# Kernel optimization log

Measured on AMD Instinct MI355X. Metric: run time of the kernel, lower is better.

## Reference

```python
import jax, jax.numpy as jnp
import numpy as np

B, S, D, H, L, F = 4, 2048, 512, 8, 4, 2048
DH = D // H
EPS = 1e-5


def setup_inputs() -> dict:
    key = jax.random.key(0)
    ks = jax.random.split(key, 16)
    sc = 0.02
    inp = {
        "turn_embeddings": jax.random.normal(ks[0], (B, S, D), jnp.float32),
        "Wqkv": jax.random.normal(ks[1], (L, 3 * D, D), jnp.float32) * sc,
        "bqkv": jnp.zeros((L, 3 * D), jnp.float32),
        "Wo": jax.random.normal(ks[2], (L, D, D), jnp.float32) * sc,
        "bo": jnp.zeros((L, D), jnp.float32),
        "W1": jax.random.normal(ks[3], (L, F, D), jnp.float32) * sc,
        "b1": jnp.zeros((L, F), jnp.float32),
        "W2": jax.random.normal(ks[4], (L, D, F), jnp.float32) * sc,
        "b2": jnp.zeros((L, D), jnp.float32),
        "ln1_g": jnp.ones((L, D), jnp.float32),
        "ln1_b": jnp.zeros((L, D), jnp.float32),
        "ln2_g": jnp.ones((L, D), jnp.float32),
        "ln2_b": jnp.zeros((L, D), jnp.float32),
        "speaker_ids": jax.random.randint(ks[5], (B, S), 0, 4, jnp.int64 if jax.config.jax_enable_x64 else jnp.int32),
    }
    return inp


def _layer_norm(x, g, b):
    mu = jnp.mean(x, axis=-1, keepdims=True)
    var = jnp.mean(jnp.square(x - mu), axis=-1, keepdims=True)
    return (x - mu) * jax.lax.rsqrt(var + EPS) * g + b


def _attention(x, Wqkv, bqkv, Wo, bo, allow):
    # x: [B,S,D]; allow: [B,1,S,S] boolean (causal & same-speaker)
    qkv = x @ Wqkv.T + bqkv                       # [B,S,3D]
    q, k, v = jnp.split(qkv, 3, axis=-1)
    q = q.reshape(x.shape[0], x.shape[1], H, DH)
    k = k.reshape(x.shape[0], x.shape[1], H, DH)
    v = v.reshape(x.shape[0], x.shape[1], H, DH)
    scores = jnp.einsum("bqhd,bkhd->bhqk", q, k) / np.sqrt(DH)
    scores = jnp.where(allow, scores, jnp.finfo(scores.dtype).min)
    p = jax.nn.softmax(scores, axis=-1)
    o = jnp.einsum("bhqk,bkhd->bqhd", p, v).reshape(x.shape[0], x.shape[1], D)
    return o @ Wo.T + bo


def reference(turn_embeddings, Wqkv, bqkv, Wo, bo, W1, b1, W2, b2,
              ln1_g, ln1_b, ln2_g, ln2_b, speaker_ids):
    Bc, Sc, _ = turn_embeddings.shape
    causal = jnp.tril(jnp.ones((Sc, Sc), bool))                 # [S,S]
    same = speaker_ids[:, :, None] == speaker_ids[:, None, :]    # [B,S,S]
    allow = (same & causal)[:, None, :, :]                       # [B,1,S,S]
    x = turn_embeddings
    for l in range(L):
        a = _attention(x, Wqkv[l], bqkv[l], Wo[l], bo[l], allow)
        x = _layer_norm(x + a, ln1_g[l], ln1_b[l])
        h = jax.nn.relu(x @ W1[l].T + b1[l]) @ W2[l].T + b2[l]
        x = _layer_norm(x + h, ln2_g[l], ln2_b[l])
    return x
```

## Files before the change

kernel.cpp:

```cpp
#include <hip/hip_runtime.h>
#include <stdint.h>

#define BN 4
#define SN 2048
#define DN 512
#define HN 8
#define LN 4
#define FN 2048
#define MN (BN * SN)
#define TD (3 * DN)

typedef __attribute__((ext_vector_type(8))) __bf16 bf16x8;
typedef __attribute__((ext_vector_type(4))) float f32x4;
typedef __attribute__((ext_vector_type(8))) unsigned short ushortx8;

static __device__ __forceinline__ unsigned short f2bf(float f) {
    return __builtin_bit_cast(unsigned short, (__bf16)f);
}
static __device__ __forceinline__ float bf2f(unsigned short h) {
    return __builtin_bit_cast(float, (uint32_t)h << 16);
}

static __device__ __forceinline__ void gload16(const void* g, void* l) {
    __builtin_amdgcn_global_load_lds(
        (const __attribute__((address_space(1))) void*)g,
        (__attribute__((address_space(3))) void*)l, 16, 0, 0);
}

__global__ __launch_bounds__(256) void k_cvt(const float* __restrict__ src,
                                             unsigned short* __restrict__ dst,
                                             int n4) {
    int i = blockIdx.x * blockDim.x + threadIdx.x;
    int stride = gridDim.x * blockDim.x;
    for (; i < n4; i += stride) {
        float4 v = ((const float4*)src)[i];
        ushort4 o;
        o.x = f2bf(v.x); o.y = f2bf(v.y); o.z = f2bf(v.z); o.w = f2bf(v.w);
        ((ushort4*)dst)[i] = o;
    }
}

template <int MODE, int BNT>
__global__ __launch_bounds__(256) void k_gemm(const unsigned short* __restrict__ A,
                                              const unsigned short* __restrict__ B,
                                              const float* __restrict__ bias,
                                              unsigned short* __restrict__ Cb,
                                              int M, int N, int K, int GX) {
    __shared__ __align__(16) unsigned short As[128][64];
    __shared__ __align__(16) unsigned short Bs[BNT][64];
    constexpr int NFR = BNT / 32;

    const int t = threadIdx.x;
    const int lane = t & 63;
    const int wid = t >> 6;
    const int wm = wid >> 1, wn = wid & 1;
    const int lr = lane & 15;
    const int lg = lane >> 4;

    const int nwg = gridDim.x;
    const int bid = blockIdx.x;
    const int swz = (bid & 7) * (nwg >> 3) + (bid >> 3);
    const int bx = swz % GX;
    const int by = swz / GX;

    const size_t rowA = (size_t)by * 128;
    const size_t rowB = (size_t)bx * BNT;
    const unsigned short* Ab = A + rowA * K;
    const unsigned short* Bb = B + rowB * K;

    const int srow = lane >> 3;
    const int sgran = (lane & 7) ^ srow;

    f32x4 acc[4][NFR] = {};

    for (int k0 = 0; k0 < K; k0 += 64) {
        __syncthreads();
#pragma unroll
        for (int j = 0; j < 4; ++j) {
            const int c = wid * 4 + j;
            const size_t goff = (size_t)(8 * c + srow) * K + k0 + sgran * 8;
            gload16(Ab + goff, &As[8 * c][0]);
        }
#pragma unroll
        for (int j = 0; j < NFR; ++j) {
            const int c = wid * NFR + j;
            const size_t goff = (size_t)(8 * c + srow) * K + k0 + sgran * 8;
            gload16(Bb + goff, &Bs[8 * c][0]);
        }
        __syncthreads();

#pragma unroll
        for (int h = 0; h < 2; ++h) {
            const int gp = (h * 4 + lg) ^ (lr & 7);
            bf16x8 af[4], bfr[NFR];
#pragma unroll
            for (int mi = 0; mi < 4; ++mi)
                af[mi] = *(const bf16x8*)&As[wm * 64 + mi * 16 + lr][gp * 8];
#pragma unroll
            for (int ni = 0; ni < NFR; ++ni)
                bfr[ni] = *(const bf16x8*)&Bs[wn * (BNT / 2) + ni * 16 + lr][gp * 8];
#pragma unroll
            for (int mi = 0; mi < 4; ++mi)
#pragma unroll
                for (int ni = 0; ni < NFR; ++ni)
                    acc[mi][ni] = __builtin_amdgcn_mfma_f32_16x16x32_bf16(
                        af[mi], bfr[ni], acc[mi][ni], 0, 0, 0);
        }
    }

    float bv[NFR];
#pragma unroll
    for (int ni = 0; ni < NFR; ++ni)
        bv[ni] = bias[(int)rowB + wn * (BNT / 2) + ni * 16 + lr];

#pragma unroll
    for (int mi = 0; mi < 4; ++mi) {
#pragma unroll
        for (int ni = 0; ni < NFR; ++ni) {
            int col = (int)rowB + wn * (BNT / 2) + ni * 16 + lr;
            int row0 = (int)rowA + wm * 64 + mi * 16 + lg * 4;
#pragma unroll
            for (int r = 0; r < 4; ++r) {
                float v = acc[mi][ni][r] + bv[ni];
                if (MODE == 2) v = fmaxf(v, 0.f);
                Cb[(size_t)(row0 + r) * N + col] = f2bf(v);
            }
        }
    }
}

__global__ __launch_bounds__(256) void k_attn(const unsigned short* __restrict__ qkv,
                                              const int* __restrict__ spk,
                                              unsigned short* __restrict__ o) {
    __shared__ __align__(16) unsigned short Ks[2][64][64];
    __shared__ __align__(16) unsigned short Vt[2][64][64];
    __shared__ __align__(16) unsigned short Ps[4][16][64];

    const int t = threadIdx.x;
    const int lane = t & 63;
    const int w = t >> 6;
    const int lr = lane & 15;
    const int lg = lane >> 4;
    const int l7 = lr & 7;

    const int wg = blockIdx.x;
    const int inner = wg >> 3;
    const int bh = 4 * (wg & 7) + (inner & 3);
    const int qtile = (SN / 64 - 1) - (inner >> 2);
    const int b = bh >> 3;
    const int h = bh & 7;
    const int qb = qtile * 64;

    const size_t base = (size_t)b * SN * TD;
    const unsigned short* kg = qkv + base + DN + h * 64;
    const unsigned short* vg = qkv + base + 2 * DN + h * 64;

    const float SCL = 0.125f * 1.4426950408889634f;
    const unsigned short* qptr = qkv + base + (size_t)(qb + w * 16 + lr) * TD + h * 64;
    bf16x8 aq0 = *(const bf16x8*)(qptr + lg * 8);
    bf16x8 aq1 = *(const bf16x8*)(qptr + 32 + lg * 8);
#pragma unroll
    for (int j = 0; j < 8; ++j) {
        aq0[j] = (__bf16)((float)aq0[j] * SCL);
        aq1[j] = (__bf16)((float)aq1[j] * SCL);
    }

    int sqr[4], qrow[4];
#pragma unroll
    for (int r = 0; r < 4; ++r) {
        qrow[r] = qb + w * 16 + lg * 4 + r;
        sqr[r] = spk[b * SN + qrow[r]];
    }

    const int kr0 = t >> 3;
    const int kgr = ((t & 7) ^ (kr0 & 7)) * 8;
    const int vrow = t & 63;
    const int vd0 = (t >> 6) * 16;

    uint4 kra = *(const uint4*)&kg[(size_t)kr0 * TD + (t & 7) * 8];
    uint4 krb = *(const uint4*)&kg[(size_t)(kr0 + 32) * TD + (t & 7) * 8];
    ushortx8 vra = *(const ushortx8*)&vg[(size_t)vrow * TD + vd0];
    ushortx8 vrb = *(const ushortx8*)&vg[(size_t)vrow * TD + vd0 + 8];
    *(uint4*)&Ks[0][kr0][kgr] = kra;
    *(uint4*)&Ks[0][kr0 + 32][kgr] = krb;
#pragma unroll
    for (int j = 0; j < 8; ++j) {
        const int vcol = (((vrow >> 3) ^ j) << 3) + (vrow & 7);
        Vt[0][vd0 + j][vcol] = vra[j];
        Vt[0][vd0 + 8 + j][vcol] = vrb[j];
    }

    float lsum[4] = {0.f, 0.f, 0.f, 0.f};
    f32x4 acc_o[4] = {};

    const int ntiles = qtile + 1;
    for (int it = 0; it < ntiles; ++it) {
        const int k0 = it * 64;
        const int cur = it & 1;
        __syncthreads();

        const bool nx = (it + 1 < ntiles);
        if (nx) {
            const int kn = k0 + 64;
            kra = *(const uint4*)&kg[(size_t)(kn + kr0) * TD + (t & 7) * 8];
            krb = *(const uint4*)&kg[(size_t)(kn + kr0 + 32) * TD + (t & 7) * 8];
            vra = *(const ushortx8*)&vg[(size_t)(kn + vrow) * TD + vd0];
            vrb = *(const ushortx8*)&vg[(size_t)(kn + vrow) * TD + vd0 + 8];
        }
        int skr[4];
#pragma unroll
        for (int ni = 0; ni < 4; ++ni) skr[ni] = spk[b * SN + k0 + 16 * ni + lr];

        f32x4 sc4[4] = {};
        __builtin_amdgcn_s_setprio(1);
#pragma unroll
        for (int ni = 0; ni < 4; ++ni) {
            bf16x8 bk0 = *(const bf16x8*)&Ks[cur][16 * ni + lr][(lg ^ l7) * 8];
            bf16x8 bk1 = *(const bf16x8*)&Ks[cur][16 * ni + lr][((lg + 4) ^ l7) * 8];
            sc4[ni] = __builtin_amdgcn_mfma_f32_16x16x32_bf16(aq0, bk0, sc4[ni], 0, 0, 0);
            sc4[ni] = __builtin_amdgcn_mfma_f32_16x16x32_bf16(aq1, bk1, sc4[ni], 0, 0, 0);
        }
        __builtin_amdgcn_s_setprio(0);

        const bool diag = (it == ntiles - 1);
#pragma unroll
        for (int ni = 0; ni < 4; ++ni) {
#pragma unroll
            for (int r = 0; r < 4; ++r) {
                bool allow = (skr[ni] == sqr[r]);
                if (diag) allow = allow && (16 * ni + lr <= w * 16 + lg * 4 + r);
                float p = allow ? __builtin_amdgcn_exp2f(sc4[ni][r]) : 0.f;
                lsum[r] += p;
                const int q7 = (lg * 4 + r) & 7;
                const int pg = ((2 * ni + (lr >> 3)) ^ q7) * 8 + l7;
                Ps[w][lg * 4 + r][pg] = f2bf(p);
            }
        }

        bf16x8 ap0 = *(const bf16x8*)&Ps[w][lr][(lg ^ l7) * 8];
        bf16x8 ap1 = *(const bf16x8*)&Ps[w][lr][((lg + 4) ^ l7) * 8];
        __builtin_amdgcn_s_setprio(1);
#pragma unroll
        for (int ni = 0; ni < 4; ++ni) {
            bf16x8 bv0 = *(const bf16x8*)&Vt[cur][16 * ni + lr][(lg ^ l7) * 8];
            bf16x8 bv1 = *(const bf16x8*)&Vt[cur][16 * ni + lr][((lg + 4) ^ l7) * 8];
            acc_o[ni] = __builtin_amdgcn_mfma_f32_16x16x32_bf16(ap0, bv0, acc_o[ni], 0, 0, 0);
            acc_o[ni] = __builtin_amdgcn_mfma_f32_16x16x32_bf16(ap1, bv1, acc_o[ni], 0, 0, 0);
        }
        __builtin_amdgcn_s_setprio(0);

        if (nx) {
            const int nb = cur ^ 1;
            *(uint4*)&Ks[nb][kr0][kgr] = kra;
            *(uint4*)&Ks[nb][kr0 + 32][kgr] = krb;
#pragma unroll
            for (int j = 0; j < 8; ++j) {
                const int vcol = (((vrow >> 3) ^ j) << 3) + (vrow & 7);
                Vt[nb][vd0 + j][vcol] = vra[j];
                Vt[nb][vd0 + 8 + j][vcol] = vrb[j];
            }
        }
    }

#pragma unroll
    for (int r = 0; r < 4; ++r) {
        float s = lsum[r];
        s += __shfl_xor(s, 1);
        s += __shfl_xor(s, 2);
        s += __shfl_xor(s, 4);
        s += __shfl_xor(s, 8);
        float inv = 1.f / s;
#pragma unroll
        for (int ni = 0; ni < 4; ++ni) {
            int d = 16 * ni + lr;
            o[(size_t)(b * SN + qrow[r]) * DN + h * 64 + d] = f2bf(acc_o[ni][r] * inv);
        }
    }
}

template <bool XF32>
__global__ __launch_bounds__(256) void k_add_ln(const void* __restrict__ xin_,
                                                const unsigned short* __restrict__ dl,
                                                const float* __restrict__ g,
                                                const float* __restrict__ bta,
                                                unsigned short* __restrict__ xb,
                                                float* __restrict__ fout) {
    const int row = blockIdx.x * 4 + (threadIdx.x >> 6);
    const int lane = threadIdx.x & 63;
    const size_t off = (size_t)row * DN + lane * 8;
    const int c0 = lane * 8;

    float v[8];
    if (XF32) {
        const float* xin = (const float*)xin_;
        float4 a0 = *(const float4*)&xin[off];
        float4 a1 = *(const float4*)&xin[off + 4];
        v[0] = a0.x; v[1] = a0.y; v[2] = a0.z; v[3] = a0.w;
        v[4] = a1.x; v[5] = a1.y; v[6] = a1.z; v[7] = a1.w;
    } else {
        ushortx8 xa = *(const ushortx8*)&((const unsigned short*)xin_)[off];
#pragma unroll
        for (int i = 0; i < 8; ++i) v[i] = bf2f(xa[i]);
    }
    ushortx8 dd = *(const ushortx8*)&dl[off];
#pragma unroll
    for (int i = 0; i < 8; ++i) v[i] += bf2f(dd[i]);

    float s1 = 0.f, s2 = 0.f;
#pragma unroll
    for (int i = 0; i < 8; ++i) { s1 += v[i]; s2 += v[i] * v[i]; }
#pragma unroll
    for (int msk = 32; msk; msk >>= 1) {
        s1 += __shfl_xor(s1, msk);
        s2 += __shfl_xor(s2, msk);
    }
    const float mean = s1 * (1.f / 512.f);
    const float var = s2 * (1.f / 512.f) - mean * mean;
    const float rs = rsqrtf(var + 1e-5f);

    float4 g0 = *(const float4*)&g[c0];
    float4 g1 = *(const float4*)&g[c0 + 4];
    float4 b0 = *(const float4*)&bta[c0];
    float4 b1 = *(const float4*)&bta[c0 + 4];
    float gg[8] = {g0.x, g0.y, g0.z, g0.w, g1.x, g1.y, g1.z, g1.w};
    float bb[8] = {b0.x, b0.y, b0.z, b0.w, b1.x, b1.y, b1.z, b1.w};

    float y[8];
    ushortx8 ub;
#pragma unroll
    for (int i = 0; i < 8; ++i) {
        y[i] = (v[i] - mean) * rs * gg[i] + bb[i];
        ub[i] = f2bf(y[i]);
    }
    *(ushortx8*)&xb[off] = ub;
    if (fout) {
        *(float4*)&fout[off] = make_float4(y[0], y[1], y[2], y[3]);
        *(float4*)&fout[off + 4] = make_float4(y[4], y[5], y[6], y[7]);
    }
}

extern "C" void kernel_launch(void* const* d_in, const int* in_sizes, int n_in,
                              void* d_out, int out_size, void* d_ws, size_t ws_size,
                              hipStream_t stream) {
    const float* te   = (const float*)d_in[0];
    const float* Wqkv = (const float*)d_in[1];
    const float* bqkv = (const float*)d_in[2];
    const float* Wo   = (const float*)d_in[3];
    const float* bo   = (const float*)d_in[4];
    const float* W1   = (const float*)d_in[5];
    const float* b1   = (const float*)d_in[6];
    const float* W2   = (const float*)d_in[7];
    const float* b2   = (const float*)d_in[8];
    const float* g1   = (const float*)d_in[9];
    const float* be1  = (const float*)d_in[10];
    const float* g2   = (const float*)d_in[11];
    const float* be2  = (const float*)d_in[12];
    const int*   spk  = (const int*)d_in[13];
    float* out = (float*)d_out;

    char* ws = (char*)d_ws;
    size_t off = 0;
    auto alloc = [&](size_t bytes) -> char* {
        char* p = ws + off;
        off += (bytes + 255) & ~(size_t)255;
        return p;
    };
    unsigned short* wqkv_b = (unsigned short*)alloc((size_t)LN * TD * DN * 2);
    unsigned short* wo_b   = (unsigned short*)alloc((size_t)LN * DN * DN * 2);
    unsigned short* w1_b   = (unsigned short*)alloc((size_t)LN * FN * DN * 2);
    unsigned short* w2_b   = (unsigned short*)alloc((size_t)LN * DN * FN * 2);
    unsigned short* xb     = (unsigned short*)alloc((size_t)MN * DN * 2);
    unsigned short* u      = (unsigned short*)alloc((size_t)MN * FN * 2);
    unsigned short* ob     = (unsigned short*)alloc((size_t)MN * DN * 2);
    unsigned short* projb  = (unsigned short*)alloc((size_t)MN * DN * 2);
    unsigned short* qkvb = u;
    unsigned short* hb   = u;

    k_cvt<<<2048, 256, 0, stream>>>(Wqkv, wqkv_b, LN * TD * DN / 4);
    k_cvt<<<2048, 256, 0, stream>>>(Wo,   wo_b,   LN * DN * DN / 4);
    k_cvt<<<2048, 256, 0, stream>>>(W1,   w1_b,   LN * FN * DN / 4);
    k_cvt<<<2048, 256, 0, stream>>>(W2,   w2_b,   LN * DN * FN / 4);
    k_cvt<<<2048, 256, 0, stream>>>(te,   xb,     MN * DN / 4);

    for (int l = 0; l < LN; ++l) {
        k_gemm<1, 128><<<(MN / 128) * (TD / 128), 256, 0, stream>>>(
            xb, wqkv_b + (size_t)l * TD * DN, bqkv + l * TD, qkvb,
            MN, TD, DN, TD / 128);
        k_attn<<<(SN / 64) * BN * HN, 256, 0, stream>>>(qkvb, spk, ob);
        k_gemm<1, 64><<<(MN / 128) * (DN / 64), 256, 0, stream>>>(
            ob, wo_b + (size_t)l * DN * DN, bo + l * DN, projb,
            MN, DN, DN, DN / 64);
        if (l == 0)
            k_add_ln<true><<<MN / 4, 256, 0, stream>>>(
                te, projb, g1 + l * DN, be1 + l * DN, xb, nullptr);
        else
            k_add_ln<false><<<MN / 4, 256, 0, stream>>>(
                xb, projb, g1 + l * DN, be1 + l * DN, xb, nullptr);
        k_gemm<2, 128><<<(MN / 128) * (FN / 128), 256, 0, stream>>>(
            xb, w1_b + (size_t)l * FN * DN, b1 + l * FN, hb,
            MN, FN, DN, FN / 128);
        k_gemm<1, 64><<<(MN / 128) * (DN / 64), 256, 0, stream>>>(
            hb, w2_b + (size_t)l * DN * FN, b2 + l * DN, projb,
            MN, DN, FN, DN / 64);
        k_add_ln<false><<<MN / 4, 256, 0, stream>>>(
            xb, projb, g2 + l * DN, be2 + l * DN, xb,
            (l == LN - 1) ? out : nullptr);
    }
    (void)in_sizes; (void)n_in; (void)out_size; (void)ws_size;
}
```

Before: 606.3 us.

## Widen attention blocks to 128 queries with 8 waves and fuse weight conversions

The attention kernel now runs 512 threads per block covering 128 query rows, so each K/V tile loaded into LDS is shared by twice as many waves, and the grid is halved. K tiles are fetched with direct global-to-LDS loads, speaker ids are cached in LDS as bytes, and waves skip key tiles that lie entirely past their causal limit. The five fp32-to-bf16 conversion launches are merged into one kernel with range dispatch. Costs include larger blocks with per-wave load imbalance on the diagonal tiles, and fewer blocks to spread across the compute units.

```diff
diff --git a/kernel.cpp b/kernel.cpp
--- a/kernel.cpp
+++ b/kernel.cpp
@@ -27,16 +27,34 @@
         (__attribute__((address_space(3))) void*)l, 16, 0, 0);
 }
 
-__global__ __launch_bounds__(256) void k_cvt(const float* __restrict__ src,
-                                             unsigned short* __restrict__ dst,
-                                             int n4) {
+__global__ __launch_bounds__(256) void k_cvt_all(const float* __restrict__ Wqkv,
+                                                 const float* __restrict__ Wo,
+                                                 const float* __restrict__ W1,
+                                                 const float* __restrict__ W2,
+                                                 const float* __restrict__ te,
+                                                 unsigned short* __restrict__ wqkv_b,
+                                                 unsigned short* __restrict__ wo_b,
+                                                 unsigned short* __restrict__ w1_b,
+                                                 unsigned short* __restrict__ w2_b,
+                                                 unsigned short* __restrict__ xb) {
+    constexpr int G0 = LN * TD * DN / 4;
+    constexpr int G1 = G0 + LN * DN * DN / 4;
+    constexpr int G2 = G1 + LN * FN * DN / 4;
+    constexpr int G3 = G2 + LN * DN * FN / 4;
+    constexpr int G4 = G3 + MN * DN / 4;
     int i = blockIdx.x * blockDim.x + threadIdx.x;
     int stride = gridDim.x * blockDim.x;
-    for (; i < n4; i += stride) {
-        float4 v = ((const float4*)src)[i];
+    for (; i < G4; i += stride) {
+        const float* s; unsigned short* d; int j;
+        if (i < G0)      { s = Wqkv; d = wqkv_b; j = i; }
+        else if (i < G1) { s = Wo;   d = wo_b;   j = i - G0; }
+        else if (i < G2) { s = W1;   d = w1_b;   j = i - G1; }
+        else if (i < G3) { s = W2;   d = w2_b;   j = i - G2; }
+        else             { s = te;   d = xb;     j = i - G3; }
+        float4 v = ((const float4*)s)[j];
         ushort4 o;
         o.x = f2bf(v.x); o.y = f2bf(v.y); o.z = f2bf(v.z); o.w = f2bf(v.w);
-        ((ushort4*)dst)[i] = o;
+        ((ushort4*)d)[j] = o;
     }
 }
 
@@ -129,12 +147,13 @@
     }
 }
 
-__global__ __launch_bounds__(256) void k_attn(const unsigned short* __restrict__ qkv,
+__global__ __launch_bounds__(512) void k_attn(const unsigned short* __restrict__ qkv,
                                               const int* __restrict__ spk,
                                               unsigned short* __restrict__ o) {
     __shared__ __align__(16) unsigned short Ks[2][64][64];
     __shared__ __align__(16) unsigned short Vt[2][64][64];
-    __shared__ __align__(16) unsigned short Ps[4][16][64];
+    __shared__ __align__(16) unsigned short Ps[8][16][64];
+    __shared__ unsigned char skb[SN];
 
     const int t = threadIdx.x;
     const int lane = t & 63;
@@ -146,14 +165,16 @@
     const int wg = blockIdx.x;
     const int inner = wg >> 3;
     const int bh = 4 * (wg & 7) + (inner & 3);
-    const int qtile = (SN / 64 - 1) - (inner >> 2);
+    const int qsuper = (SN / 128 - 1) - (inner >> 2);
     const int b = bh >> 3;
     const int h = bh & 7;
-    const int qb = qtile * 64;
+    const int qb = qsuper * 128;
 
     const size_t base = (size_t)b * SN * TD;
     const unsigned short* kg = qkv + base + DN + h * 64;
     const unsigned short* vg = qkv + base + 2 * DN + h * 64;
+
+    for (int i = t; i < SN; i += 512) skb[i] = (unsigned char)spk[b * SN + i];
 
     const float SCL = 0.125f * 1.4426950408889634f;
     const unsigned short* qptr = qkv + base + (size_t)(qb + w * 16 + lr) * TD + h * 64;
@@ -172,28 +193,24 @@
         sqr[r] = spk[b * SN + qrow[r]];
     }
 
-    const int kr0 = t >> 3;
-    const int kgr = ((t & 7) ^ (kr0 & 7)) * 8;
+    const int krow = t >> 3;
+    const int kgran = (t & 7) ^ (krow & 7);
     const int vrow = t & 63;
-    const int vd0 = (t >> 6) * 16;
-
-    uint4 kra = *(const uint4*)&kg[(size_t)kr0 * TD + (t & 7) * 8];
-    uint4 krb = *(const uint4*)&kg[(size_t)(kr0 + 32) * TD + (t & 7) * 8];
+    const int vd0 = w * 8;
+
+    gload16(kg + (size_t)krow * TD + kgran * 8, &Ks[0][w * 8][0]);
     ushortx8 vra = *(const ushortx8*)&vg[(size_t)vrow * TD + vd0];
-    ushortx8 vrb = *(const ushortx8*)&vg[(size_t)vrow * TD + vd0 + 8];
-    *(uint4*)&Ks[0][kr0][kgr] = kra;
-    *(uint4*)&Ks[0][kr0 + 32][kgr] = krb;
 #pragma unroll
     for (int j = 0; j < 8; ++j) {
         const int vcol = (((vrow >> 3) ^ j) << 3) + (vrow & 7);
         Vt[0][vd0 + j][vcol] = vra[j];
-        Vt[0][vd0 + 8 + j][vcol] = vrb[j];
     }
 
     float lsum[4] = {0.f, 0.f, 0.f, 0.f};
     f32x4 acc_o[4] = {};
 
-    const int ntiles = qtile + 1;
+    const int ntiles = qb / 64 + 2;
+    const int qlast = qb + w * 16 + 15;
     for (int it = 0; it < ntiles; ++it) {
         const int k0 = it * 64;
         const int cur = it & 1;
@@ -202,62 +219,60 @@
         const bool nx = (it + 1 < ntiles);
         if (nx) {
             const int kn = k0 + 64;
-            kra = *(const uint4*)&kg[(size_t)(kn + kr0) * TD + (t & 7) * 8];
-            krb = *(const uint4*)&kg[(size_t)(kn + kr0 + 32) * TD + (t & 7) * 8];
+            gload16(kg + (size_t)(kn + krow) * TD + kgran * 8, &Ks[cur ^ 1][w * 8][0]);
             vra = *(const ushortx8*)&vg[(size_t)(kn + vrow) * TD + vd0];
-            vrb = *(const ushortx8*)&vg[(size_t)(kn + vrow) * TD + vd0 + 8];
-        }
-        int skr[4];
-#pragma unroll
-        for (int ni = 0; ni < 4; ++ni) skr[ni] = spk[b * SN + k0 + 16 * ni + lr];
-
-        f32x4 sc4[4] = {};
-        __builtin_amdgcn_s_setprio(1);
-#pragma unroll
-        for (int ni = 0; ni < 4; ++ni) {
-            bf16x8 bk0 = *(const bf16x8*)&Ks[cur][16 * ni + lr][(lg ^ l7) * 8];
-            bf16x8 bk1 = *(const bf16x8*)&Ks[cur][16 * ni + lr][((lg + 4) ^ l7) * 8];
-            sc4[ni] = __builtin_amdgcn_mfma_f32_16x16x32_bf16(aq0, bk0, sc4[ni], 0, 0, 0);
-            sc4[ni] = __builtin_amdgcn_mfma_f32_16x16x32_bf16(aq1, bk1, sc4[ni], 0, 0, 0);
-        }
-        __builtin_amdgcn_s_setprio(0);
-
-        const bool diag = (it == ntiles - 1);
-#pragma unroll
-        for (int ni = 0; ni < 4; ++ni) {
-#pragma unroll
-            for (int r = 0; r < 4; ++r) {
-                bool allow = (skr[ni] == sqr[r]);
-                if (diag) allow = allow && (16 * ni + lr <= w * 16 + lg * 4 + r);
-                float p = allow ? __builtin_amdgcn_exp2f(sc4[ni][r]) : 0.f;
-                lsum[r] += p;
-                const int q7 = (lg * 4 + r) & 7;
-                const int pg = ((2 * ni + (lr >> 3)) ^ q7) * 8 + l7;
-                Ps[w][lg * 4 + r][pg] = f2bf(p);
+        }
+
+        if (k0 <= qlast) {
+            int skr[4];
+#pragma unroll
+            for (int ni = 0; ni < 4; ++ni) skr[ni] = skb[k0 + 16 * ni + lr];
+
+            f32x4 sc4[4] = {};
+            __builtin_amdgcn_s_setprio(1);
+#pragma unroll
+            for (int ni = 0; ni < 4; ++ni) {
+                bf16x8 bk0 = *(const bf16x8*)&Ks[cur][16 * ni + lr][(lg ^ l7) * 8];
+                bf16x8 bk1 = *(const bf16x8*)&Ks[cur][16 * ni + lr][((lg + 4) ^ l7) * 8];
+                sc4[ni] = __builtin_amdgcn_mfma_f32_16x16x32_bf16(aq0, bk0, sc4[ni], 0, 0, 0);
+                sc4[ni] = __builtin_amdgcn_mfma_f32_16x16x32_bf16(aq1, bk1, sc4[ni], 0, 0, 0);
             }
-        }
-
-        bf16x8 ap0 = *(const bf16x8*)&Ps[w][lr][(lg ^ l7) * 8];
-        bf16x8 ap1 = *(const bf16x8*)&Ps[w][lr][((lg + 4) ^ l7) * 8];
-        __builtin_amdgcn_s_setprio(1);
-#pragma unroll
-        for (int ni = 0; ni < 4; ++ni) {
-            bf16x8 bv0 = *(const bf16x8*)&Vt[cur][16 * ni + lr][(lg ^ l7) * 8];
-            bf16x8 bv1 = *(const bf16x8*)&Vt[cur][16 * ni + lr][((lg + 4) ^ l7) * 8];
-            acc_o[ni] = __builtin_amdgcn_mfma_f32_16x16x32_bf16(ap0, bv0, acc_o[ni], 0, 0, 0);
-            acc_o[ni] = __builtin_amdgcn_mfma_f32_16x16x32_bf16(ap1, bv1, acc_o[ni], 0, 0, 0);
-        }
-        __builtin_amdgcn_s_setprio(0);
+            __builtin_amdgcn_s_setprio(0);
+
+            const bool needC = (k0 + 63 >= qb + w * 16);
+#pragma unroll
+            for (int ni = 0; ni < 4; ++ni) {
+#pragma unroll
+                for (int r = 0; r < 4; ++r) {
+                    bool allow = (skr[ni] == sqr[r]);
+                    if (needC) allow = allow && (k0 + 16 * ni + lr <= qrow[r]);
+                    float p = allow ? __builtin_amdgcn_exp2f(sc4[ni][r]) : 0.f;
+                    lsum[r] += p;
+                    const int q7 = (lg * 4 + r) & 7;
+                    const int pg = ((2 * ni + (lr >> 3)) ^ q7) * 8 + l7;
+                    Ps[w][lg * 4 + r][pg] = f2bf(p);
+                }
+            }
+
+            bf16x8 ap0 = *(const bf16x8*)&Ps[w][lr][(lg ^ l7) * 8];
+            bf16x8 ap1 = *(const bf16x8*)&Ps[w][lr][((lg + 4) ^ l7) * 8];
+            __builtin_amdgcn_s_setprio(1);
+#pragma unroll
+            for (int ni = 0; ni < 4; ++ni) {
+                bf16x8 bv0 = *(const bf16x8*)&Vt[cur][16 * ni + lr][(lg ^ l7) * 8];
+                bf16x8 bv1 = *(const bf16x8*)&Vt[cur][16 * ni + lr][((lg + 4) ^ l7) * 8];
+                acc_o[ni] = __builtin_amdgcn_mfma_f32_16x16x32_bf16(ap0, bv0, acc_o[ni], 0, 0, 0);
+                acc_o[ni] = __builtin_amdgcn_mfma_f32_16x16x32_bf16(ap1, bv1, acc_o[ni], 0, 0, 0);
+            }
+            __builtin_amdgcn_s_setprio(0);
+        }
 
         if (nx) {
             const int nb = cur ^ 1;
-            *(uint4*)&Ks[nb][kr0][kgr] = kra;
-            *(uint4*)&Ks[nb][kr0 + 32][kgr] = krb;
 #pragma unroll
             for (int j = 0; j < 8; ++j) {
                 const int vcol = (((vrow >> 3) ^ j) << 3) + (vrow & 7);
                 Vt[nb][vd0 + j][vcol] = vra[j];
-                Vt[nb][vd0 + 8 + j][vcol] = vrb[j];
             }
         }
     }
@@ -376,17 +391,14 @@
     unsigned short* qkvb = u;
     unsigned short* hb   = u;
 
-    k_cvt<<<2048, 256, 0, stream>>>(Wqkv, wqkv_b, LN * TD * DN / 4);
-    k_cvt<<<2048, 256, 0, stream>>>(Wo,   wo_b,   LN * DN * DN / 4);
-    k_cvt<<<2048, 256, 0, stream>>>(W1,   w1_b,   LN * FN * DN / 4);
-    k_cvt<<<2048, 256, 0, stream>>>(W2,   w2_b,   LN * DN * FN / 4);
-    k_cvt<<<2048, 256, 0, stream>>>(te,   xb,     MN * DN / 4);
+    k_cvt_all<<<2048, 256, 0, stream>>>(Wqkv, Wo, W1, W2, te,
+                                        wqkv_b, wo_b, w1_b, w2_b, xb);
 
     for (int l = 0; l < LN; ++l) {
         k_gemm<1, 128><<<(MN / 128) * (TD / 128), 256, 0, stream>>>(
             xb, wqkv_b + (size_t)l * TD * DN, bqkv + l * TD, qkvb,
             MN, TD, DN, TD / 128);
-        k_attn<<<(SN / 64) * BN * HN, 256, 0, stream>>>(qkvb, spk, ob);
+        k_attn<<<(SN / 128) * BN * HN, 512, 0, stream>>>(qkvb, spk, ob);
         k_gemm<1, 64><<<(MN / 128) * (DN / 64), 256, 0, stream>>>(
             ob, wo_b + (size_t)l * DN * DN, bo + l * DN, projb,
             MN, DN, DN, DN / 64);
```

New measurement: 670.2 us. +10.5%, slower.
